# Kernel optimization log

Hardware: AMD Instinct MI355X
Metric: run time of the kernel (lower is better)

Reference implementation:

```python
import jax, jax.numpy as jnp
import numpy as np

NUM_CLASSES = 4
PROTO_MOMENTUM = 0.9
CONF_THRESH = 0.8
LAMBDA_INTRA = 1.0
LAMBDA_INTER = 0.1
MARGIN_M = 1.0


def setup_inputs() -> dict:
    key = jax.random.key(0)
    k1, k2, k3, k4 = jax.random.split(key, 4)
    B, C, H, W, D = 2, 64, 96, 96, 96
    K = NUM_CLASSES + 1
    feat = jax.random.normal(k1, (B, C, H, W, D), dtype=jnp.float32)
    # softmax predictions; sharpen logits so a realistic fraction exceeds conf_thresh
    logits = jax.random.normal(k2, (B, K, H, W, D), dtype=jnp.float32)
    pred = jax.nn.softmax(4.0 * logits, axis=1)
    label = jax.random.randint(k3, (B, 1, H, W, D), 0, K, dtype=jnp.int32)
    is_labelled = jnp.ones((B,), dtype=bool)
    prototypes = jax.random.normal(k4, (NUM_CLASSES, C), dtype=jnp.float32)
    return {"feat": feat, "pred": pred, "label": label,
            "is_labelled": is_labelled, "prototypes": prototypes}


def reference(feat, pred, label, is_labelled, prototypes):
    B, C, H, W, D = feat.shape
    K = pred.shape[1]
    N = B * H * W * D
    dt = feat.dtype

    # flatten spatial dims: (N, C), (N, K), (N,)
    feat_flat = jnp.transpose(feat, (0, 2, 3, 4, 1)).reshape(-1, C)
    pred_flat = jnp.transpose(pred, (0, 2, 3, 4, 1)).reshape(-1, K)
    label_flat = label.reshape(-1)
    is_lab_flat = jnp.broadcast_to(is_labelled[:, None], (B, H * W * D)).reshape(-1)

    # high-confidence mask
    pred_conf = jnp.max(pred_flat, axis=1)
    pred_class = jnp.argmax(pred_flat, axis=1).astype(jnp.int32)
    conf_mask = (pred_conf > CONF_THRESH) & (pred_class > 0)
    conf_mask = conf_mask & ((pred_class == label_flat) | ~is_lab_flat)

    # segmented per-class mean over masked voxels (single scatter-add pass)
    seg = jnp.where(conf_mask, pred_class - 1, NUM_CLASSES)  # dummy bucket for masked-out
    maskf = conf_mask.astype(dt)
    cnt = jax.ops.segment_sum(maskf, seg, num_segments=NUM_CLASSES + 1)[:NUM_CLASSES]
    sums = jax.ops.segment_sum(feat_flat * maskf[:, None], seg,
                               num_segments=NUM_CLASSES + 1)[:NUM_CLASSES]
    class_mean = sums / jnp.maximum(cnt, 1.0)[:, None]
    present = cnt > 0

    # EMA prototype update (buffer update: no grad through the batch means)
    proto_new = jnp.where(
        present[:, None],
        PROTO_MOMENTUM * prototypes + (1.0 - PROTO_MOMENTUM) * jax.lax.stop_gradient(class_mean),
        prototypes,
    )

    # intra-class compactness: mean over masked voxels of ||f_i - mu_{c_i}||^2
    proto_per_vox = proto_new[jnp.clip(pred_class - 1, 0, NUM_CLASSES - 1)]  # (N, C)
    d2 = jnp.sum((feat_flat - proto_per_vox) ** 2, axis=1)
    n_valid = jnp.sum(maskf)
    loss_intra = jnp.sum(maskf * d2) / jnp.maximum(n_valid, 1.0)

    # inter-class separation: hinge on pairwise prototype distances (upper triangle)
    diff = proto_new[:, None, :] - proto_new[None, :, :]
    dist = jnp.sqrt(jnp.sum(diff ** 2, axis=2) + 1e-12)
    triu = jnp.triu(jnp.ones((NUM_CLASSES, NUM_CLASSES), dtype=bool), k=1)
    viol = jnp.maximum(MARGIN_M - dist, 0.0) ** 2
    n_pairs = NUM_CLASSES * (NUM_CLASSES - 1) // 2
    loss_inter = jnp.sum(jnp.where(triu, viol, 0.0)) / n_pairs

    loss_total = LAMBDA_INTRA * loss_intra + LAMBDA_INTER * loss_inter
    return loss_total, loss_intra, loss_inter, proto_new
```

## Files before the change

kernel.cpp:

```cpp
#include <hip/hip_runtime.h>

#define HWD 884736
#define KCLS 5
#define CCH 64
#define NC 4

constexpr int PLANE4 = HWD / 4;
constexpr int GRP_B  = HWD / 4;
constexpr int NBLKM  = 2 * GRP_B / 256;
constexpr int NPART  = 16;
constexpr int PARTSZ = 272;
constexpr int MASK_OFF_BYTES = 32768;

constexpr int ITER = 27;
constexpr int SEGG = 256 * ITER;
constexpr int NSEG = PLANE4 / SEGG;
constexpr int NBLKS = 2 * CCH * NSEG;

__global__ __launch_bounds__(256) void pm_zero(float* __restrict__ part) {
    const int n = NPART * PARTSZ;
    for (int i = threadIdx.x; i < n; i += 256) part[i] = 0.f;
}

__global__ __launch_bounds__(256) void pm_mask(
    const float* __restrict__ pred, const int* __restrict__ label,
    const unsigned char* __restrict__ is_lab,
    unsigned int* __restrict__ mask, float* __restrict__ part)
{
    __shared__ float lcnt[NC];
    const int t = threadIdx.x;
    if (t < NC) lcnt[t] = 0.f;
    __syncthreads();

    const int g = blockIdx.x * 256 + t;
    const int b = (blockIdx.x >= NBLKM / 2);
    const int gg = g - b * GRP_B;

    const float4* pb = (const float4*)(pred + (size_t)b * KCLS * HWD) + gg;
    float4 pk[KCLS];
    #pragma unroll
    for (int k = 0; k < KCLS; ++k) pk[k] = pb[(size_t)k * PLANE4];
    const int4 lb = ((const int4*)(label + (size_t)b * HWD))[gg];
    const bool lab = is_lab[b] != 0;

    unsigned int wd = 0;
    #pragma unroll
    for (int j = 0; j < 4; ++j) {
        float best = -1.f; int c = 0;
        #pragma unroll
        for (int k = 0; k < KCLS; ++k) {
            float v = ((const float*)&pk[k])[j];
            if (v > best) { best = v; c = k; }
        }
        const int lj = ((const int*)&lb)[j];
        const bool m = (best > 0.8f) & (c > 0) & ((c == lj) | (!lab));
        if (m) {
            wd |= (4u | (unsigned)(c - 1)) << (3 * j);
            atomicAdd(&lcnt[c - 1], 1.f);
        }
    }
    mask[g] = wd;
    __syncthreads();
    if (t < NC) {
        float c = lcnt[t];
        if (c != 0.f)
            atomicAdd(&part[(size_t)(blockIdx.x & (NPART - 1)) * PARTSZ + 256 + t], c);
    }
}

__global__ __launch_bounds__(256) void pm_sweep(
    const float* __restrict__ feat, const unsigned int* __restrict__ mask,
    float* __restrict__ part)
{
    const int t = threadIdx.x, l = t & 63;
    const int bi = blockIdx.x;
    const int b   = bi >> 11;
    const int rem = bi & 2047;
    const int c   = rem >> 5;
    const int seg = rem & 31;
    const int g0  = seg * SEGG;

    const float4* fb = (const float4*)(feat + (size_t)(b * CCH + c) * HWD);
    const unsigned int* mb = mask + (size_t)b * PLANE4;

    float s0 = 0.f, s1 = 0.f, s2 = 0.f, s3 = 0.f;
    float q0 = 0.f, q1 = 0.f, q2 = 0.f, q3 = 0.f;

    #pragma unroll 3
    for (int i = 0; i < ITER; ++i) {
        const int gg = g0 + i * 256 + t;
        const unsigned int wm = mb[gg];
        const float4 f = fb[gg];
        #pragma unroll
        for (int j = 0; j < 4; ++j) {
            const int bits = (wm >> (3 * j)) & 7;
            const float v = ((const float*)&f)[j];
            const float v2 = v * v;
            if (bits == 4) { s0 += v; q0 += v2; }
            if (bits == 5) { s1 += v; q1 += v2; }
            if (bits == 6) { s2 += v; q2 += v2; }
            if (bits == 7) { s3 += v; q3 += v2; }
        }
    }

    #pragma unroll
    for (int o = 1; o < 64; o <<= 1) {
        s0 += __shfl_xor(s0, o); s1 += __shfl_xor(s1, o);
        s2 += __shfl_xor(s2, o); s3 += __shfl_xor(s3, o);
        q0 += __shfl_xor(q0, o); q1 += __shfl_xor(q1, o);
        q2 += __shfl_xor(q2, o); q3 += __shfl_xor(q3, o);
    }

    float* dst = part + (size_t)(bi & (NPART - 1)) * PARTSZ;
    if (l < NC) {
        const float sv = (l == 0) ? s0 : (l == 1) ? s1 : (l == 2) ? s2 : s3;
        if (sv != 0.f) atomicAdd(&dst[l * 64 + c], sv);
    } else if (l < 2 * NC) {
        const int k = l - NC;
        const float qv = (k == 0) ? q0 : (k == 1) ? q1 : (k == 2) ? q2 : q3;
        if (qv != 0.f) atomicAdd(&dst[260 + k], qv);
    }
}

__global__ __launch_bounds__(256) void pm_pass2(
    const float* __restrict__ part, const float* __restrict__ proto,
    float* __restrict__ out)
{
    __shared__ float scnt[NC], ssq[NC], smu[NC * CCH], sred[4];
    __shared__ float s_intra;
    const int t = threadIdx.x;
    const int q = t >> 6;

    float s = 0.f;
    #pragma unroll
    for (int p = 0; p < NPART; ++p) s += part[p * PARTSZ + t];
    if (t < 2 * NC) {
        float a = 0.f;
        #pragma unroll
        for (int p = 0; p < NPART; ++p) a += part[p * PARTSZ + 256 + t];
        if (t < NC) scnt[t] = a; else ssq[t - NC] = a;
    }
    __syncthreads();

    const float cq = scnt[q];
    const float mean = s / fmaxf(cq, 1.f);
    const float pold = proto[t];
    const float mu = (cq > 0.f) ? 0.9f * pold + 0.1f * mean : pold;
    out[3 + t] = mu;
    smu[t] = mu;

    float pi = -2.f * s * mu + cq * mu * mu;
    #pragma unroll
    for (int o = 1; o < 64; o <<= 1) pi += __shfl_xor(pi, o);
    if ((t & 63) == 0) sred[t >> 6] = pi;
    __syncthreads();

    if (t == 0) {
        float num = sred[0] + sred[1] + sred[2] + sred[3]
                  + ssq[0] + ssq[1] + ssq[2] + ssq[3];
        float nv = scnt[0] + scnt[1] + scnt[2] + scnt[3];
        s_intra = num / fmaxf(nv, 1.f);
    }
    __syncthreads();

    if (t < 64) {
        const int pi_[6] = {0, 0, 0, 1, 1, 2};
        const int pj_[6] = {1, 2, 3, 2, 3, 3};
        float acc = 0.f;
        #pragma unroll
        for (int e = 0; e < 6; ++e) {
            float d = smu[pi_[e] * 64 + t] - smu[pj_[e] * 64 + t];
            float d2 = d * d;
            #pragma unroll
            for (int o = 1; o < 64; o <<= 1) d2 += __shfl_xor(d2, o);
            float dist = sqrtf(d2 + 1e-12f);
            float vv = fmaxf(1.f - dist, 0.f);
            acc += vv * vv;
        }
        if (t == 0) {
            float li = acc / 6.f;
            out[0] = s_intra + 0.1f * li;
            out[1] = s_intra;
            out[2] = li;
        }
    }
}

extern "C" void kernel_launch(void* const* d_in, const int* in_sizes, int n_in,
                              void* d_out, int out_size, void* d_ws, size_t ws_size,
                              hipStream_t stream) {
    const float* feat         = (const float*)d_in[0];
    const float* pred         = (const float*)d_in[1];
    const int* label          = (const int*)d_in[2];
    const unsigned char* ilab = (const unsigned char*)d_in[3];
    const float* proto        = (const float*)d_in[4];
    float* out                = (float*)d_out;
    float* part               = (float*)d_ws;
    unsigned int* mask        = (unsigned int*)((char*)d_ws + MASK_OFF_BYTES);

    hipLaunchKernelGGL(pm_zero,  dim3(1),     dim3(256), 0, stream, part);
    hipLaunchKernelGGL(pm_mask,  dim3(NBLKM), dim3(256), 0, stream,
                       pred, label, ilab, mask, part);
    hipLaunchKernelGGL(pm_sweep, dim3(NBLKS), dim3(256), 0, stream, feat, mask, part);
    hipLaunchKernelGGL(pm_pass2, dim3(1),     dim3(256), 0, stream, part, proto, out);
}
```

Before: 105.8 us.

## Replace atomic partial accumulation with per-block partial writes and drop zero kernel

Each mask and sweep block now writes its per-class counts and sums to its own slot in a partials buffer instead of atomically adding into 16 shared partitions. This removes the zero-init launch and atomic contention. The final single-block kernel reduces all block partials itself. Loads of pred, label and feat also become nontemporal to avoid polluting cache with streamed data. The trade-off is more serial reduction work in the one-block final kernel, which now reads about 4096x8 sweep partials and 6912 count entries.

```diff
diff --git a/kernel.cpp b/kernel.cpp
--- a/kernel.cpp
+++ b/kernel.cpp
@@ -5,27 +5,26 @@
 #define CCH 64
 #define NC 4
 
+typedef float  f32x4 __attribute__((ext_vector_type(4)));
+typedef int    i32x4 __attribute__((ext_vector_type(4)));
+
 constexpr int PLANE4 = HWD / 4;
 constexpr int GRP_B  = HWD / 4;
 constexpr int NBLKM  = 2 * GRP_B / 256;
-constexpr int NPART  = 16;
-constexpr int PARTSZ = 272;
-constexpr int MASK_OFF_BYTES = 32768;
 
 constexpr int ITER = 27;
 constexpr int SEGG = 256 * ITER;
 constexpr int NSEG = PLANE4 / SEGG;
 constexpr int NBLKS = 2 * CCH * NSEG;
 
-__global__ __launch_bounds__(256) void pm_zero(float* __restrict__ part) {
-    const int n = NPART * PARTSZ;
-    for (int i = threadIdx.x; i < n; i += 256) part[i] = 0.f;
-}
+constexpr size_t CNT_OFF  = 0;
+constexpr size_t SWP_OFF  = 32768;
+constexpr size_t MASK_OFF = 163840;
 
 __global__ __launch_bounds__(256) void pm_mask(
     const float* __restrict__ pred, const int* __restrict__ label,
     const unsigned char* __restrict__ is_lab,
-    unsigned int* __restrict__ mask, float* __restrict__ part)
+    unsigned int* __restrict__ mask, float4* __restrict__ cntP)
 {
     __shared__ float lcnt[NC];
     const int t = threadIdx.x;
@@ -36,11 +35,11 @@
     const int b = (blockIdx.x >= NBLKM / 2);
     const int gg = g - b * GRP_B;
 
-    const float4* pb = (const float4*)(pred + (size_t)b * KCLS * HWD) + gg;
-    float4 pk[KCLS];
-    #pragma unroll
-    for (int k = 0; k < KCLS; ++k) pk[k] = pb[(size_t)k * PLANE4];
-    const int4 lb = ((const int4*)(label + (size_t)b * HWD))[gg];
+    const f32x4* pb = (const f32x4*)(pred + (size_t)b * KCLS * HWD) + gg;
+    f32x4 pk[KCLS];
+    #pragma unroll
+    for (int k = 0; k < KCLS; ++k) pk[k] = __builtin_nontemporal_load(pb + (size_t)k * PLANE4);
+    const i32x4 lb = __builtin_nontemporal_load((const i32x4*)(label + (size_t)b * HWD) + gg);
     const bool lab = is_lab[b] != 0;
 
     unsigned int wd = 0;
@@ -49,10 +48,10 @@
         float best = -1.f; int c = 0;
         #pragma unroll
         for (int k = 0; k < KCLS; ++k) {
-            float v = ((const float*)&pk[k])[j];
+            float v = pk[k][j];
             if (v > best) { best = v; c = k; }
         }
-        const int lj = ((const int*)&lb)[j];
+        const int lj = lb[j];
         const bool m = (best > 0.8f) & (c > 0) & ((c == lj) | (!lab));
         if (m) {
             wd |= (4u | (unsigned)(c - 1)) << (3 * j);
@@ -61,18 +60,15 @@
     }
     mask[g] = wd;
     __syncthreads();
-    if (t < NC) {
-        float c = lcnt[t];
-        if (c != 0.f)
-            atomicAdd(&part[(size_t)(blockIdx.x & (NPART - 1)) * PARTSZ + 256 + t], c);
-    }
+    if (t == 0) cntP[blockIdx.x] = make_float4(lcnt[0], lcnt[1], lcnt[2], lcnt[3]);
 }
 
 __global__ __launch_bounds__(256) void pm_sweep(
     const float* __restrict__ feat, const unsigned int* __restrict__ mask,
-    float* __restrict__ part)
+    float* __restrict__ partS)
 {
-    const int t = threadIdx.x, l = t & 63;
+    __shared__ float ws8[4][8];
+    const int t = threadIdx.x, w = t >> 6, l = t & 63;
     const int bi = blockIdx.x;
     const int b   = bi >> 11;
     const int rem = bi & 2047;
@@ -80,7 +76,7 @@
     const int seg = rem & 31;
     const int g0  = seg * SEGG;
 
-    const float4* fb = (const float4*)(feat + (size_t)(b * CCH + c) * HWD);
+    const f32x4* fb = (const f32x4*)(feat + (size_t)(b * CCH + c) * HWD);
     const unsigned int* mb = mask + (size_t)b * PLANE4;
 
     float s0 = 0.f, s1 = 0.f, s2 = 0.f, s3 = 0.f;
@@ -90,11 +86,11 @@
     for (int i = 0; i < ITER; ++i) {
         const int gg = g0 + i * 256 + t;
         const unsigned int wm = mb[gg];
-        const float4 f = fb[gg];
+        const f32x4 f = __builtin_nontemporal_load(fb + gg);
         #pragma unroll
         for (int j = 0; j < 4; ++j) {
             const int bits = (wm >> (3 * j)) & 7;
-            const float v = ((const float*)&f)[j];
+            const float v = f[j];
             const float v2 = v * v;
             if (bits == 4) { s0 += v; q0 += v2; }
             if (bits == 5) { s1 += v; q1 += v2; }
@@ -110,35 +106,65 @@
         q0 += __shfl_xor(q0, o); q1 += __shfl_xor(q1, o);
         q2 += __shfl_xor(q2, o); q3 += __shfl_xor(q3, o);
     }
-
-    float* dst = part + (size_t)(bi & (NPART - 1)) * PARTSZ;
-    if (l < NC) {
-        const float sv = (l == 0) ? s0 : (l == 1) ? s1 : (l == 2) ? s2 : s3;
-        if (sv != 0.f) atomicAdd(&dst[l * 64 + c], sv);
-    } else if (l < 2 * NC) {
-        const int k = l - NC;
-        const float qv = (k == 0) ? q0 : (k == 1) ? q1 : (k == 2) ? q2 : q3;
-        if (qv != 0.f) atomicAdd(&dst[260 + k], qv);
-    }
+    if (l < 8) {
+        const float v = (l == 0) ? s0 : (l == 1) ? s1 : (l == 2) ? s2 : (l == 3) ? s3
+                      : (l == 4) ? q0 : (l == 5) ? q1 : (l == 6) ? q2 : q3;
+        ws8[w][l] = v;
+    }
+    __syncthreads();
+    if (t < 8)
+        partS[(size_t)bi * 8 + t] = ws8[0][t] + ws8[1][t] + ws8[2][t] + ws8[3][t];
 }
 
 __global__ __launch_bounds__(256) void pm_pass2(
-    const float* __restrict__ part, const float* __restrict__ proto,
-    float* __restrict__ out)
+    const float* __restrict__ partS, const float4* __restrict__ cntP,
+    const float* __restrict__ proto, float* __restrict__ out)
 {
     __shared__ float scnt[NC], ssq[NC], smu[NC * CCH], sred[4];
+    __shared__ float4 sc4[4];
+    __shared__ float q4[4][4];
     __shared__ float s_intra;
-    const int t = threadIdx.x;
+    const int t = threadIdx.x, w = t >> 6, l = t & 63;
     const int q = t >> 6;
+    const int c = t & 63;
+
+    {
+        float4 a = make_float4(0.f, 0.f, 0.f, 0.f);
+        for (int i = t; i < NBLKM; i += 256) {
+            const float4 v = cntP[i];
+            a.x += v.x; a.y += v.y; a.z += v.z; a.w += v.w;
+        }
+        #pragma unroll
+        for (int o = 1; o < 64; o <<= 1) {
+            a.x += __shfl_xor(a.x, o); a.y += __shfl_xor(a.y, o);
+            a.z += __shfl_xor(a.z, o); a.w += __shfl_xor(a.w, o);
+        }
+        if (l == 0) sc4[w] = a;
+    }
 
     float s = 0.f;
-    #pragma unroll
-    for (int p = 0; p < NPART; ++p) s += part[p * PARTSZ + t];
-    if (t < 2 * NC) {
-        float a = 0.f;
-        #pragma unroll
-        for (int p = 0; p < NPART; ++p) a += part[p * PARTSZ + 256 + t];
-        if (t < NC) scnt[t] = a; else ssq[t - NC] = a;
+    #pragma unroll 4
+    for (int b = 0; b < 2; ++b)
+        for (int seg = 0; seg < 32; ++seg)
+            s += partS[(size_t)((b * 2048) + (c * 32) + seg) * 8 + q];
+
+    {
+        const int g = t >> 2, kk = t & 3;
+        float qq = 0.f;
+        #pragma unroll 4
+        for (int j = 0; j < 64; ++j)
+            qq += partS[(size_t)(g + 64 * j) * 8 + 4 + kk];
+        #pragma unroll
+        for (int o = 4; o < 64; o <<= 1) qq += __shfl_xor(qq, o);
+        if (l < 4) q4[w][l] = qq;
+    }
+    __syncthreads();
+    if (t < NC) {
+        const float4 c0 = sc4[0], c1 = sc4[1], c2 = sc4[2], c3 = sc4[3];
+        const float cv = ((const float*)&c0)[t] + ((const float*)&c1)[t]
+                       + ((const float*)&c2)[t] + ((const float*)&c3)[t];
+        scnt[t] = cv;
+        ssq[t] = q4[0][t] + q4[1][t] + q4[2][t] + q4[3][t];
     }
     __syncthreads();
 
@@ -195,12 +221,14 @@
     const unsigned char* ilab = (const unsigned char*)d_in[3];
     const float* proto        = (const float*)d_in[4];
     float* out                = (float*)d_out;
-    float* part               = (float*)d_ws;
-    unsigned int* mask        = (unsigned int*)((char*)d_ws + MASK_OFF_BYTES);
-
-    hipLaunchKernelGGL(pm_zero,  dim3(1),     dim3(256), 0, stream, part);
+
+    float4* cntP       = (float4*)((char*)d_ws + CNT_OFF);
+    float* partS       = (float*)((char*)d_ws + SWP_OFF);
+    unsigned int* mask = (unsigned int*)((char*)d_ws + MASK_OFF);
+
     hipLaunchKernelGGL(pm_mask,  dim3(NBLKM), dim3(256), 0, stream,
-                       pred, label, ilab, mask, part);
-    hipLaunchKernelGGL(pm_sweep, dim3(NBLKS), dim3(256), 0, stream, feat, mask, part);
-    hipLaunchKernelGGL(pm_pass2, dim3(1),     dim3(256), 0, stream, part, proto, out);
-}
+                       pred, label, ilab, mask, cntP);
+    hipLaunchKernelGGL(pm_sweep, dim3(NBLKS), dim3(256), 0, stream, feat, mask, partS);
+    hipLaunchKernelGGL(pm_pass2, dim3(1),     dim3(256), 0, stream,
+                       partS, cntP, proto, out);
+}
```

New measurement: 98.44 us. -7.0%, faster.
